# Performance work log

Measured on AMD Instinct MI355X. Metric: run time of the kernel, lower is better.

## Reference

```python
import jax, jax.numpy as jnp
import numpy as np
import math

N_HEADS = 16
HEAD_DIM = 128  # dim=2048 / 16


def _rope(t, cos, sin):
    # t: [B, S, H, hd]; cos/sin: [1, S, hd//2]
    B, S, H, hd = t.shape
    tr = t.reshape(B, S, H, hd // 2, 2)
    te, to = tr[..., 0], tr[..., 1]
    c = cos[:, :, None, :]
    s = sin[:, :, None, :]
    oe = te * c - to * s
    oo = te * s + to * c
    return jnp.stack([oe, oo], axis=-1).reshape(B, S, H, hd)


def setup_inputs() -> dict:
    key = jax.random.key(0)
    ks = jax.random.split(key, 5)
    B, S, D = 2, 2048, 2048
    hd = HEAD_DIM
    scale = 1.0 / math.sqrt(D)
    x = jax.random.normal(ks[0], (B, S, D), dtype=jnp.float32)
    wq = jax.random.normal(ks[1], (D, D), dtype=jnp.float32) * scale
    wk = jax.random.normal(ks[2], (D, D), dtype=jnp.float32) * scale
    wv = jax.random.normal(ks[3], (D, D), dtype=jnp.float32) * scale
    wo = jax.random.normal(ks[4], (D, D), dtype=jnp.float32) * scale
    # true RoPE angles: freqs = base^(-2i/hd), angles = pos * freqs
    base = 10000.0
    inv_freq = 1.0 / (base ** (np.arange(0, hd, 2, dtype=np.float32) / hd))  # [hd//2]
    pos = np.arange(S, dtype=np.float32)
    ang = pos[:, None] * inv_freq[None, :]  # [S, hd//2]
    pos_cos = jnp.asarray(np.cos(ang))[None]  # [1, S, hd//2]
    pos_sin = jnp.asarray(np.sin(ang))[None]
    return {"x": x, "wq": wq, "wk": wk, "wv": wv, "wo": wo,
            "pos_cos": pos_cos, "pos_sin": pos_sin}


def reference(x, wq, wk, wv, wo, pos_cos, pos_sin):
    B, S, D = x.shape
    H, hd = N_HEADS, HEAD_DIM
    # nn.Linear: y = x @ W.T
    q = (x @ wq.T).reshape(B, S, H, hd)
    k = (x @ wk.T).reshape(B, S, H, hd)
    v = (x @ wv.T).reshape(B, S, H, hd)
    q = _rope(q, pos_cos, pos_sin)
    k = _rope(k, pos_cos, pos_sin)
    # naive full attention, softmax in fp32 (as original)
    scores = jnp.einsum('bqhd,bkhd->bhqk', q, k) / math.sqrt(hd)
    probs = jax.nn.softmax(scores.astype(jnp.float32), axis=-1).astype(q.dtype)
    out = jnp.einsum('bhqk,bkhd->bqhd', probs, v).reshape(B, S, H * hd)
    return out @ wo.T
```

## Files before the change

kernel.cpp:

```cpp
#include <hip/hip_runtime.h>
#include <hip/hip_bf16.h>

typedef __attribute__((ext_vector_type(8))) short short8;
typedef __attribute__((ext_vector_type(4))) float f32x4;
typedef __attribute__((ext_vector_type(8))) unsigned short ushort8v;

#define AS_GLOBAL __attribute__((address_space(1)))
#define AS_LDS    __attribute__((address_space(3)))

__device__ __forceinline__ void async_ld16(const void* src, void* lds) {
  __builtin_amdgcn_global_load_lds((const AS_GLOBAL unsigned int*)src,
                                   (AS_LDS unsigned int*)lds, 16, 0, 0);
}

__device__ __forceinline__ unsigned short f2bf(float f) {
  unsigned int u = __float_as_uint(f);
  u = (u + 0x7fffu + ((u >> 16) & 1u)) >> 16;
  return (unsigned short)u;
}

__global__ void cvt_bf16(const float* __restrict__ x,  const float* __restrict__ wq,
                         const float* __restrict__ wk, const float* __restrict__ wvv,
                         const float* __restrict__ wo,
                         unsigned short* __restrict__ xb,  unsigned short* __restrict__ wqb,
                         unsigned short* __restrict__ wkb, unsigned short* __restrict__ wvb,
                         unsigned short* __restrict__ wob)
{
  const int NX = 8388608, NW = 4194304;
  const int total = (NX + 4 * NW) >> 3;
  for (int v = blockIdx.x * blockDim.x + threadIdx.x; v < total;
       v += gridDim.x * blockDim.x) {
    int base = v << 3;
    const float* src; unsigned short* dst; int off;
    if (base < NX) { src = x; dst = xb; off = base; }
    else {
      int t = base - NX; int w = t >> 22; off = t & (NW - 1);
      src = (w == 0) ? wq : (w == 1) ? wk : (w == 2) ? wvv : wo;
      dst = (w == 0) ? wqb : (w == 1) ? wkb : (w == 2) ? wvb : wob;
    }
    float4 f0 = *(const float4*)(src + off);
    float4 f1 = *(const float4*)(src + off + 4);
    ushort8v o;
    o[0] = f2bf(f0.x); o[1] = f2bf(f0.y); o[2] = f2bf(f0.z); o[3] = f2bf(f0.w);
    o[4] = f2bf(f1.x); o[5] = f2bf(f1.y); o[6] = f2bf(f1.z); o[7] = f2bf(f1.w);
    *(ushort8v*)(dst + off) = o;
  }
}

#define BM 128
#define BN 128
#define BKT 64

template<int MODE>
__global__ __launch_bounds__(256, 3) void gemm_bt(
    const short* __restrict__ A, const short* __restrict__ B,
    void* __restrict__ C, int M, int N, int K,
    const float* __restrict__ pcos, const float* __restrict__ psin)
{
  __shared__ short As[BM * BKT];
  __shared__ short Bs[BN * BKT];

  const int tid  = threadIdx.x;
  const int lane = tid & 63;
  const int wv   = tid >> 6;
  const int wr   = (wv >> 1) << 6;
  const int wc   = (wv & 1) << 6;
  const int l15  = lane & 15;
  const int lg   = lane >> 4;

  const int nbn = N >> 7;
  const int nwg = gridDim.x;
  int id = blockIdx.x;
  id = (id & 7) * (nwg >> 3) + (id >> 3);
  const int m0 = (id / nbn) << 7;
  const int n0 = (id % nbn) << 7;

  f32x4 acc[4][4] = {};

  for (int kt = 0; kt < K; kt += BKT) {
    __syncthreads();
#pragma unroll
    for (int i = 0; i < 4; ++i) {
      int c = i * 256 + tid;
      int r = c >> 3;
      int colb = (c & 7) << 4;
      int scol = colb ^ ((r & 7) << 4);
      async_ld16((const char*)A + (((size_t)(m0 + r) * K + kt) << 1) + scol,
                 (char*)As + c * 16);
    }
#pragma unroll
    for (int i = 0; i < 4; ++i) {
      int c = i * 256 + tid;
      int r = c >> 3;
      int colb = (c & 7) << 4;
      int scol = colb ^ ((r & 7) << 4);
      async_ld16((const char*)B + (((size_t)(n0 + r) * K + kt) << 1) + scol,
                 (char*)Bs + c * 16);
    }
    __syncthreads();

#pragma unroll
    for (int kk = 0; kk < 2; ++kk) {
      const int kb = (kk << 6) + (lg << 4);
      short8 af[4], bf[4];
#pragma unroll
      for (int mi = 0; mi < 4; ++mi) {
        int row = wr + (mi << 4) + l15;
        af[mi] = *(const short8*)((const char*)As + (row << 7) + (kb ^ ((row & 7) << 4)));
      }
#pragma unroll
      for (int ni = 0; ni < 4; ++ni) {
        int row = wc + (ni << 4) + l15;
        bf[ni] = *(const short8*)((const char*)Bs + (row << 7) + (kb ^ ((row & 7) << 4)));
      }
#pragma unroll
      for (int mi = 0; mi < 4; ++mi)
#pragma unroll
        for (int ni = 0; ni < 4; ++ni)
          acc[mi][ni] = __builtin_amdgcn_mfma_f32_16x16x32_bf16(
              af[mi], bf[ni], acc[mi][ni], 0, 0, 0);
    }
  }

#pragma unroll
  for (int mi = 0; mi < 4; ++mi) {
#pragma unroll
    for (int ni = 0; ni < 4; ++ni) {
      const int col  = n0 + wc + (ni << 4) + l15;
      const int row0 = m0 + wr + (mi << 4) + (lg << 2);
      if (MODE == 0) {
#pragma unroll
        for (int r = 0; r < 4; ++r)
          ((unsigned short*)C)[(size_t)(row0 + r) * N + col] = f2bf(acc[mi][ni][r]);
      } else if (MODE == 1) {
        const int d = col & 127;
        const int j = d >> 1;
#pragma unroll
        for (int r = 0; r < 4; ++r) {
          int s = (row0 + r) & 2047;
          float cv = pcos[(s << 6) + j];
          float sv = psin[(s << 6) + j];
          float v  = acc[mi][ni][r];
          float pv = __shfl_xor(v, 1, 64);
          float o  = (d & 1) ? (pv * sv + v * cv) : (v * cv - pv * sv);
          ((unsigned short*)C)[(size_t)(row0 + r) * N + col] = f2bf(o);
        }
      } else if (MODE == 2) {
        const int h = col >> 7, d = col & 127;
        const int b = row0 >> 11, s = row0 & 2047;
        unsigned long long pk =
              (unsigned long long)f2bf(acc[mi][ni][0])
            | ((unsigned long long)f2bf(acc[mi][ni][1]) << 16)
            | ((unsigned long long)f2bf(acc[mi][ni][2]) << 32)
            | ((unsigned long long)f2bf(acc[mi][ni][3]) << 48);
        *(unsigned long long*)((unsigned short*)C +
            (((((size_t)b << 4) + h) << 7) + d) * 2048 + s) = pk;
      } else {
#pragma unroll
        for (int r = 0; r < 4; ++r)
          ((float*)C)[(size_t)(row0 + r) * N + col] = acc[mi][ni][r];
      }
    }
  }
}

__global__ __launch_bounds__(256, 2) void flash_fwd(
    const short* __restrict__ Q, const short* __restrict__ Kg,
    const short* __restrict__ VT, unsigned short* __restrict__ O)
{
  __shared__ short Ks[128 * 128];
  __shared__ short Vs[128 * 128];
  __shared__ short Ps[4 * 16 * 128];

  const int tid  = threadIdx.x;
  const int lane = tid & 63;
  const int wv   = tid >> 6;
  const int l15  = lane & 15;
  const int lg   = lane >> 4;

  const int bh   = blockIdx.y;
  const int b    = bh >> 4;
  const int q0   = blockIdx.x << 6;
  const int hcol = (bh & 15) << 7;

  short8 qf[4];
  {
    const size_t qoff = ((size_t)((b << 11) + q0 + (wv << 4) + l15) << 11) + hcol;
#pragma unroll
    for (int ks = 0; ks < 4; ++ks)
      qf[ks] = *(const short8*)(Q + qoff + (ks << 5) + (lg << 3));
  }

  f32x4 oacc[8] = {};
  float mrow[4] = {-3e38f, -3e38f, -3e38f, -3e38f};
  float lrow[4] = {0.f, 0.f, 0.f, 0.f};
  const float cl2 = 0.1275313940154099f;

  char* const pbase = (char*)Ps + (wv << 12);

  for (int kv0 = 0; kv0 < 2048; kv0 += 128) {
    __syncthreads();
#pragma unroll
    for (int i = 0; i < 8; ++i) {
      int c = i * 256 + tid;
      int r = c >> 4;
      int colb = (c & 15) << 4;
      int scol = colb ^ ((r & 15) << 4);
      async_ld16((const char*)Kg +
                     (((size_t)((b << 11) + kv0 + r) << 11) + hcol) * 2 + scol,
                 (char*)Ks + c * 16);
    }
#pragma unroll
    for (int i = 0; i < 8; ++i) {
      int c = i * 256 + tid;
      int r = c >> 4;
      int colb = (c & 15) << 4;
      int scol = colb ^ ((r & 15) << 4);
      async_ld16((const char*)VT +
                     (((((size_t)bh << 7) + r) << 11) + kv0) * 2 + scol,
                 (char*)Vs + c * 16);
    }
    __syncthreads();

    f32x4 sc[8] = {};
#pragma unroll
    for (int ks = 0; ks < 4; ++ks) {
      const int kb = (ks << 6) + (lg << 4);
#pragma unroll
      for (int nt = 0; nt < 8; ++nt) {
        const int row = (nt << 4) + l15;
        short8 kf = *(const short8*)((const char*)Ks + (row << 8) + (kb ^ ((row & 15) << 4)));
        sc[nt] = __builtin_amdgcn_mfma_f32_16x16x32_bf16(qf[ks], kf, sc[nt], 0, 0, 0);
      }
    }

#pragma unroll
    for (int r = 0; r < 4; ++r) {
      float mx = sc[0][r];
#pragma unroll
      for (int nt = 1; nt < 8; ++nt) mx = fmaxf(mx, sc[nt][r]);
#pragma unroll
      for (int m = 1; m <= 8; m <<= 1) mx = fmaxf(mx, __shfl_xor(mx, m, 64));
      float mnew  = fmaxf(mrow[r], mx);
      float alpha = __builtin_amdgcn_exp2f((mrow[r] - mnew) * cl2);
      mrow[r] = mnew;
      lrow[r] *= alpha;
#pragma unroll
      for (int nt = 0; nt < 8; ++nt) oacc[nt][r] *= alpha;
    }

    float psum[4] = {0.f, 0.f, 0.f, 0.f};
#pragma unroll
    for (int nt = 0; nt < 8; ++nt) {
#pragma unroll
      for (int r = 0; r < 4; ++r) {
        float p = __builtin_amdgcn_exp2f((sc[nt][r] - mrow[r]) * cl2);
        psum[r] += p;
        const int row  = (lg << 2) + r;
        const int colb = ((nt << 4) + l15) << 1;
        *(unsigned short*)(pbase + (row << 8) + (colb ^ ((row & 15) << 4))) = f2bf(p);
      }
    }
#pragma unroll
    for (int r = 0; r < 4; ++r) {
      float s = psum[r];
#pragma unroll
      for (int m = 1; m <= 8; m <<= 1) s += __shfl_xor(s, m, 64);
      lrow[r] += s;
    }

#pragma unroll
    for (int ks = 0; ks < 4; ++ks) {
      const int kb = (ks << 6) + (lg << 4);
      short8 pf = *(const short8*)(pbase + (l15 << 8) + (kb ^ ((l15 & 15) << 4)));
#pragma unroll
      for (int nt = 0; nt < 8; ++nt) {
        const int row = (nt << 4) + l15;
        short8 vf = *(const short8*)((const char*)Vs + (row << 8) + (kb ^ ((row & 15) << 4)));
        oacc[nt] = __builtin_amdgcn_mfma_f32_16x16x32_bf16(pf, vf, oacc[nt], 0, 0, 0);
      }
    }
  }

  float inv[4];
#pragma unroll
  for (int r = 0; r < 4; ++r) inv[r] = 1.f / lrow[r];
#pragma unroll
  for (int nt = 0; nt < 8; ++nt) {
#pragma unroll
    for (int r = 0; r < 4; ++r) {
      const int srow = q0 + (wv << 4) + (lg << 2) + r;
      O[((size_t)((b << 11) + srow) << 11) + hcol + (nt << 4) + l15] =
          f2bf(oacc[nt][r] * inv[r]);
    }
  }
}

extern "C" void kernel_launch(void* const* d_in, const int* in_sizes, int n_in,
                              void* d_out, int out_size, void* d_ws, size_t ws_size,
                              hipStream_t stream)
{
  (void)in_sizes; (void)n_in; (void)out_size; (void)ws_size;
  const float* x    = (const float*)d_in[0];
  const float* wq   = (const float*)d_in[1];
  const float* wk   = (const float*)d_in[2];
  const float* wv   = (const float*)d_in[3];
  const float* wo   = (const float*)d_in[4];
  const float* pcos = (const float*)d_in[5];
  const float* psin = (const float*)d_in[6];

  char* ws = (char*)d_ws;
  short* xb  = (short*)(ws);
  short* wqb = (short*)(ws + 16777216);
  short* wkb = (short*)(ws + 25165824);
  short* wvb = (short*)(ws + 33554432);
  short* wob = (short*)(ws + 41943040);
  short* Qr  = (short*)(ws + 50331648);
  short* Kr  = (short*)(ws + 67108864);
  short* VT  = (short*)(ws + 83886080);
  short* At  = xb;

  cvt_bf16<<<2048, 256, 0, stream>>>(x, wq, wk, wv, wo,
      (unsigned short*)xb, (unsigned short*)wqb, (unsigned short*)wkb,
      (unsigned short*)wvb, (unsigned short*)wob);

  gemm_bt<1><<<512, 256, 0, stream>>>(xb, wqb, Qr, 4096, 2048, 2048, pcos, psin);
  gemm_bt<1><<<512, 256, 0, stream>>>(xb, wkb, Kr, 4096, 2048, 2048, pcos, psin);
  gemm_bt<2><<<512, 256, 0, stream>>>(xb, wvb, VT, 4096, 2048, 2048, nullptr, nullptr);

  flash_fwd<<<dim3(32, 32), 256, 0, stream>>>(Qr, Kr, VT, (unsigned short*)At);

  gemm_bt<3><<<512, 256, 0, stream>>>(At, wob, d_out, 4096, 2048, 2048, nullptr, nullptr);
}
```

Before: 442.6 us.

## Rewrite flash attention with 32x32 MFMA, double-buffered KV, register-resident P

Replaces the flash attention kernel with a 512-thread version that processes 256 query rows per block using 32x32x16 MFMAs and computes S transposed (K as A operand). KV tiles of 64 are double-buffered in LDS with async global-to-LDS loads overlapping compute. P stays in registers, packed to bf16 with v_cvt_pk and exchanged across half-waves via shuffles, removing the LDS round trip for P. Adds lazy max rescaling that only rescales when the row max grows by more than a threshold. This risks higher register pressure and fewer blocks (256) across the GPU.

```diff
diff --git a/kernel.cpp b/kernel.cpp
--- a/kernel.cpp
+++ b/kernel.cpp
@@ -3,7 +3,9 @@
 
 typedef __attribute__((ext_vector_type(8))) short short8;
 typedef __attribute__((ext_vector_type(4))) float f32x4;
+typedef __attribute__((ext_vector_type(16))) float f32x16;
 typedef __attribute__((ext_vector_type(8))) unsigned short ushort8v;
+typedef __attribute__((ext_vector_type(4))) unsigned int u32x4;
 
 #define AS_GLOBAL __attribute__((address_space(1)))
 #define AS_LDS    __attribute__((address_space(3)))
@@ -164,134 +166,167 @@
   }
 }
 
-__global__ __launch_bounds__(256, 2) void flash_fwd(
+__global__ __launch_bounds__(512, 2) void flash_fwd2(
     const short* __restrict__ Q, const short* __restrict__ Kg,
     const short* __restrict__ VT, unsigned short* __restrict__ O)
 {
-  __shared__ short Ks[128 * 128];
-  __shared__ short Vs[128 * 128];
-  __shared__ short Ps[4 * 16 * 128];
-
-  const int tid  = threadIdx.x;
+  __shared__ short Ks[2][64 * 128];
+  __shared__ short Vs[2][128 * 64];
+
+  const int tid = threadIdx.x;
   const int lane = tid & 63;
-  const int wv   = tid >> 6;
-  const int l15  = lane & 15;
-  const int lg   = lane >> 4;
+  const int w   = tid >> 6;
+  const int l31 = lane & 31;
+  const int hi  = lane >> 5;
 
   const int bh   = blockIdx.y;
   const int b    = bh >> 4;
-  const int q0   = blockIdx.x << 6;
+  const int q0   = blockIdx.x << 8;
   const int hcol = (bh & 15) << 7;
 
-  short8 qf[4];
+  short8 qf[8];
   {
-    const size_t qoff = ((size_t)((b << 11) + q0 + (wv << 4) + l15) << 11) + hcol;
-#pragma unroll
-    for (int ks = 0; ks < 4; ++ks)
-      qf[ks] = *(const short8*)(Q + qoff + (ks << 5) + (lg << 3));
-  }
-
-  f32x4 oacc[8] = {};
-  float mrow[4] = {-3e38f, -3e38f, -3e38f, -3e38f};
-  float lrow[4] = {0.f, 0.f, 0.f, 0.f};
+    const short* qp = Q + (((size_t)((b << 11) + q0 + (w << 5) + l31)) << 11)
+                        + hcol + (hi << 3);
+#pragma unroll
+    for (int dk = 0; dk < 8; ++dk)
+      qf[dk] = *(const short8*)(qp + (dk << 4));
+  }
+
+  const char* kS0 = (const char*)Kg +
+      (((((size_t)(b << 11)) + (tid >> 4)) << 11) + hcol) * 2 +
+      (((tid & 15) << 4) ^ (((tid >> 4) & 15) << 4));
+  const char* kS1 = (const char*)Kg +
+      (((((size_t)(b << 11)) + 32 + (tid >> 4)) << 11) + hcol) * 2 +
+      (((tid & 15) << 4) ^ (((tid >> 4) & 15) << 4));
+  const char* vS0 = (const char*)VT +
+      (((size_t)((bh << 7) + (tid >> 3))) << 12) +
+      (((tid & 7) << 4) ^ (((tid >> 3) & 7) << 4));
+  const char* vS1 = vS0 + ((size_t)64 << 12);
+
+#define STAGE(t, bf) do {                                              \
+    size_t ko = (size_t)(t) * 262144; int vo = (t) * 128;              \
+    async_ld16(kS0 + ko, (char*)Ks[bf] + tid * 16);                    \
+    async_ld16(kS1 + ko, (char*)Ks[bf] + (tid + 512) * 16);            \
+    async_ld16(vS0 + vo, (char*)Vs[bf] + tid * 16);                    \
+    async_ld16(vS1 + vo, (char*)Vs[bf] + (tid + 512) * 16);            \
+  } while (0)
+
+  f32x16 oacc[4] = {};
+  float M = -3e38f, l = 0.f;
   const float cl2 = 0.1275313940154099f;
 
-  char* const pbase = (char*)Ps + (wv << 12);
-
-  for (int kv0 = 0; kv0 < 2048; kv0 += 128) {
-    __syncthreads();
-#pragma unroll
-    for (int i = 0; i < 8; ++i) {
-      int c = i * 256 + tid;
-      int r = c >> 4;
-      int colb = (c & 15) << 4;
-      int scol = colb ^ ((r & 15) << 4);
-      async_ld16((const char*)Kg +
-                     (((size_t)((b << 11) + kv0 + r) << 11) + hcol) * 2 + scol,
-                 (char*)Ks + c * 16);
-    }
-#pragma unroll
-    for (int i = 0; i < 8; ++i) {
-      int c = i * 256 + tid;
-      int r = c >> 4;
-      int colb = (c & 15) << 4;
-      int scol = colb ^ ((r & 15) << 4);
-      async_ld16((const char*)VT +
-                     (((((size_t)bh << 7) + r) << 11) + kv0) * 2 + scol,
-                 (char*)Vs + c * 16);
-    }
-    __syncthreads();
-
-    f32x4 sc[8] = {};
+  STAGE(0, 0);
+  int cur = 0;
+
+  const int kxor = (l31 & 15) << 4;
+
+  for (int t = 0; t < 32; ++t) {
+    __builtin_amdgcn_s_barrier();
+    asm volatile("" ::: "memory");
+    if (t < 31) {
+      STAGE(t + 1, cur ^ 1);
+      asm volatile("s_waitcnt vmcnt(4)" ::: "memory");
+    } else {
+      asm volatile("s_waitcnt vmcnt(0)" ::: "memory");
+    }
+    __builtin_amdgcn_s_barrier();
+    asm volatile("" ::: "memory");
+
+    const char* kb = (const char*)Ks[cur];
+    const char* vb = (const char*)Vs[cur];
+
+    f32x16 s0 = {}, s1 = {};
+#pragma unroll
+    for (int dk = 0; dk < 8; ++dk) {
+      const int cb = ((dk << 5) + (hi << 4)) ^ kxor;
+      short8 kf0 = *(const short8*)(kb + (l31 << 8) + cb);
+      short8 kf1 = *(const short8*)(kb + ((32 + l31) << 8) + cb);
+      s0 = __builtin_amdgcn_mfma_f32_32x32x16_bf16(kf0, qf[dk], s0, 0, 0, 0);
+      s1 = __builtin_amdgcn_mfma_f32_32x32x16_bf16(kf1, qf[dk], s1, 0, 0, 0);
+    }
+
+    float tmax = s0[0];
+#pragma unroll
+    for (int r = 1; r < 16; ++r) tmax = fmaxf(tmax, s0[r]);
+#pragma unroll
+    for (int r = 0; r < 16; ++r) tmax = fmaxf(tmax, s1[r]);
+    tmax = fmaxf(tmax, __shfl_xor(tmax, 32, 64));
+    tmax *= cl2;
+    if (!__all(tmax <= M + 8.f)) {
+      float mnew = fmaxf(M, tmax);
+      float alpha = __builtin_amdgcn_exp2f(M - mnew);
+      M = mnew;
+      l *= alpha;
+#pragma unroll
+      for (int nd = 0; nd < 4; ++nd) oacc[nd] = oacc[nd] * alpha;
+    }
+    float psum = 0.f;
+#pragma unroll
+    for (int r = 0; r < 16; ++r) {
+      float p = __builtin_amdgcn_exp2f(s0[r] * cl2 - M);
+      s0[r] = p; psum += p;
+    }
+#pragma unroll
+    for (int r = 0; r < 16; ++r) {
+      float p = __builtin_amdgcn_exp2f(s1[r] * cl2 - M);
+      s1[r] = p; psum += p;
+    }
+    psum += __shfl_xor(psum, 32, 64);
+    l += psum;
+
 #pragma unroll
     for (int ks = 0; ks < 4; ++ks) {
-      const int kb = (ks << 6) + (lg << 4);
-#pragma unroll
-      for (int nt = 0; nt < 8; ++nt) {
-        const int row = (nt << 4) + l15;
-        short8 kf = *(const short8*)((const char*)Ks + (row << 8) + (kb ^ ((row & 15) << 4)));
-        sc[nt] = __builtin_amdgcn_mfma_f32_16x16x32_bf16(qf[ks], kf, sc[nt], 0, 0, 0);
-      }
-    }
-
-#pragma unroll
-    for (int r = 0; r < 4; ++r) {
-      float mx = sc[0][r];
-#pragma unroll
-      for (int nt = 1; nt < 8; ++nt) mx = fmaxf(mx, sc[nt][r]);
-#pragma unroll
-      for (int m = 1; m <= 8; m <<= 1) mx = fmaxf(mx, __shfl_xor(mx, m, 64));
-      float mnew  = fmaxf(mrow[r], mx);
-      float alpha = __builtin_amdgcn_exp2f((mrow[r] - mnew) * cl2);
-      mrow[r] = mnew;
-      lrow[r] *= alpha;
-#pragma unroll
-      for (int nt = 0; nt < 8; ++nt) oacc[nt][r] *= alpha;
-    }
-
-    float psum[4] = {0.f, 0.f, 0.f, 0.f};
-#pragma unroll
-    for (int nt = 0; nt < 8; ++nt) {
-#pragma unroll
-      for (int r = 0; r < 4; ++r) {
-        float p = __builtin_amdgcn_exp2f((sc[nt][r] - mrow[r]) * cl2);
-        psum[r] += p;
-        const int row  = (lg << 2) + r;
-        const int colb = ((nt << 4) + l15) << 1;
-        *(unsigned short*)(pbase + (row << 8) + (colb ^ ((row & 15) << 4))) = f2bf(p);
-      }
-    }
-#pragma unroll
-    for (int r = 0; r < 4; ++r) {
-      float s = psum[r];
-#pragma unroll
-      for (int m = 1; m <= 8; m <<= 1) s += __shfl_xor(s, m, 64);
-      lrow[r] += s;
-    }
-
-#pragma unroll
-    for (int ks = 0; ks < 4; ++ks) {
-      const int kb = (ks << 6) + (lg << 4);
-      short8 pf = *(const short8*)(pbase + (l15 << 8) + (kb ^ ((l15 & 15) << 4)));
-#pragma unroll
-      for (int nt = 0; nt < 8; ++nt) {
-        const int row = (nt << 4) + l15;
-        short8 vf = *(const short8*)((const char*)Vs + (row << 8) + (kb ^ ((row & 15) << 4)));
-        oacc[nt] = __builtin_amdgcn_mfma_f32_16x16x32_bf16(pf, vf, oacc[nt], 0, 0, 0);
-      }
-    }
-  }
-
-  float inv[4];
-#pragma unroll
-  for (int r = 0; r < 4; ++r) inv[r] = 1.f / lrow[r];
-#pragma unroll
-  for (int nt = 0; nt < 8; ++nt) {
-#pragma unroll
-    for (int r = 0; r < 4; ++r) {
-      const int srow = q0 + (wv << 4) + (lg << 2) + r;
-      O[((size_t)((b << 11) + srow) << 11) + hcol + (nt << 4) + l15] =
-          f2bf(oacc[nt][r] * inv[r]);
+      const int base = (ks & 1) << 3;
+      float p0, p1, p2, p3, p4, p5, p6, p7;
+      if (ks < 2) {
+        p0 = s0[base + 0]; p1 = s0[base + 1]; p2 = s0[base + 2]; p3 = s0[base + 3];
+        p4 = s0[base + 4]; p5 = s0[base + 5]; p6 = s0[base + 6]; p7 = s0[base + 7];
+      } else {
+        p0 = s1[base + 0]; p1 = s1[base + 1]; p2 = s1[base + 2]; p3 = s1[base + 3];
+        p4 = s1[base + 4]; p5 = s1[base + 5]; p6 = s1[base + 6]; p7 = s1[base + 7];
+      }
+      unsigned int X, Y, Z, W;
+      asm("v_cvt_pk_bf16_f32 %0, %1, %2" : "=v"(X) : "v"(p0), "v"(p1));
+      asm("v_cvt_pk_bf16_f32 %0, %1, %2" : "=v"(Y) : "v"(p2), "v"(p3));
+      asm("v_cvt_pk_bf16_f32 %0, %1, %2" : "=v"(Z) : "v"(p4), "v"(p5));
+      asm("v_cvt_pk_bf16_f32 %0, %1, %2" : "=v"(W) : "v"(p6), "v"(p7));
+      unsigned int SX = (unsigned int)__shfl_xor((int)X, 32, 64);
+      unsigned int SY = (unsigned int)__shfl_xor((int)Y, 32, 64);
+      unsigned int SZ = (unsigned int)__shfl_xor((int)Z, 32, 64);
+      unsigned int SW = (unsigned int)__shfl_xor((int)W, 32, 64);
+      u32x4 pw;
+      pw[0] = hi ? SZ : X;
+      pw[1] = hi ? SW : Y;
+      pw[2] = hi ? Z  : SX;
+      pw[3] = hi ? W  : SY;
+      short8 pa = __builtin_bit_cast(short8, pw);
+#pragma unroll
+      for (int nd = 0; nd < 4; ++nd) {
+        const int row = (nd << 5) + l31;
+        short8 vf = *(const short8*)(vb + (row << 7) +
+                     (((ks << 5) + (hi << 4)) ^ ((row & 7) << 4)));
+        oacc[nd] = __builtin_amdgcn_mfma_f32_32x32x16_bf16(pa, vf, oacc[nd], 0, 0, 0);
+      }
+    }
+    cur ^= 1;
+  }
+#undef STAGE
+
+  const float linv = 1.f / l;
+  float lr[16];
+#pragma unroll
+  for (int r = 0; r < 16; ++r)
+    lr[r] = __shfl(linv, (r & 3) + ((r >> 2) << 3) + (hi << 2), 64);
+
+  const size_t orow0 = (size_t)((b << 11) + q0 + (w << 5));
+#pragma unroll
+  for (int nd = 0; nd < 4; ++nd) {
+#pragma unroll
+    for (int r = 0; r < 16; ++r) {
+      const int crow = (r & 3) + ((r >> 2) << 3) + (hi << 2);
+      O[((orow0 + crow) << 11) + hcol + (nd << 5) + l31] =
+          f2bf(oacc[nd][r] * lr[r]);
     }
   }
 }
@@ -328,7 +363,7 @@
   gemm_bt<1><<<512, 256, 0, stream>>>(xb, wkb, Kr, 4096, 2048, 2048, pcos, psin);
   gemm_bt<2><<<512, 256, 0, stream>>>(xb, wvb, VT, 4096, 2048, 2048, nullptr, nullptr);
 
-  flash_fwd<<<dim3(32, 32), 256, 0, stream>>>(Qr, Kr, VT, (unsigned short*)At);
+  flash_fwd2<<<dim3(8, 32), 512, 0, stream>>>(Qr, Kr, VT, (unsigned short*)At);
 
   gemm_bt<3><<<512, 256, 0, stream>>>(At, wob, d_out, 4096, 2048, 2048, nullptr, nullptr);
 }
```

After: 379.5 us. -14.3%, faster.
